# Optimization experiments

Hardware: AMD Instinct MI355X
Metric: run time of the kernel (lower is better)

The kernel has to match this reference:

```python
import jax, jax.numpy as jnp
import numpy as np
import math

N, E, F, H = 8000, 64000, 64, 10
C = F  # out_channels == in_channels in Drug's RAGCN
INV_SQRT_F = 1.0 / math.sqrt(F)


def _glorot(key, shape):
    lim = math.sqrt(6.0 / (shape[0] + shape[1]))
    return jax.random.uniform(key, shape, jnp.float32, -lim, lim)


def setup_inputs() -> dict:
    key = jax.random.key(0)
    ks = jax.random.split(key, 16)
    x = jax.random.normal(ks[0], (N, F), jnp.float32)
    edge_attr = jax.random.normal(ks[1], (E, F), jnp.float32)
    # directed edges with no self loops (module removes them before adding its own)
    src = jax.random.randint(ks[2], (E,), 0, N)
    off = jax.random.randint(ks[3], (E,), 1, N)
    dst = (src + off) % N
    edge_index = jnp.stack([src, dst]).astype(jnp.int32)
    return {
        'x': x,
        'edge_index': edge_index,
        'edge_attr': edge_attr,
        'W_src': _glorot(ks[4], (F, H * C)),
        'Wnq': _glorot(ks[5], (F, F)),
        'Wnk': _glorot(ks[6], (F, F)),
        'Wnv': _glorot(ks[7], (F, F)),
        'Weq': _glorot(ks[8], (F, F)),
        'Wev': _glorot(ks[9], (F, F)),
        'Wek': _glorot(ks[10], (F, F)),
        'W4': _glorot(ks[11], (2 * F, F)),
        'W5': _glorot(ks[12], (F, F)),
        'g1': jnp.ones((F,), jnp.float32),
        'b1': jnp.zeros((F,), jnp.float32),
        'g2': jnp.ones((F,), jnp.float32),
        'b2': jnp.zeros((F,), jnp.float32),
        'bias': jnp.zeros((H * C,), jnp.float32),
    }


def _layernorm(v, g, b):  # torch LayerNorm, eps=0, affine, biased variance
    mu = jnp.mean(v, axis=-1, keepdims=True)
    var = jnp.mean((v - mu) ** 2, axis=-1, keepdims=True)
    return (v - mu) * jax.lax.rsqrt(var) * g + b


def reference(x, edge_index, edge_attr, W_src, Wnq, Wnk, Wnv, Weq, Wev, Wek,
              W4, W5, g1, b1, g2, b2, bias):
    src, dst = edge_index[0], edge_index[1]
    # add_self_loops with fill_value='mean': loop attr = mean of incoming edge_attr
    deg = jax.ops.segment_sum(jnp.ones((E,), x.dtype), dst, num_segments=N)
    loop_attr = jax.ops.segment_sum(edge_attr, dst, num_segments=N) / jnp.maximum(deg, 1.0)[:, None]
    loops = jnp.arange(N, dtype=src.dtype)
    s = jnp.concatenate([src, loops])                  # [Et] edge source index
    ea = jnp.concatenate([edge_attr, loop_attr], 0)    # [Et, F]

    x_src = (x @ W_src).reshape(N, H, C)               # [N, H, C]
    x_j = x_src[s]                                     # gather: [Et, H, C]

    node_K = x_j @ Wnk
    node_V = x_j @ Wnv
    node_Q = x_src @ Wnq
    edge_K = ea @ Weq   # naming follows source: w_e_q feeds edge_K etc.
    edge_V = ea @ Wev
    edge_Q = ea @ Wek

    K_s = jax.ops.segment_sum(node_K + edge_K[:, None, :], s, num_segments=N)
    V_s = jax.ops.segment_sum(node_V + edge_V[:, None, :], s, num_segments=N)
    Q_s = jax.ops.segment_sum(edge_Q, s, num_segments=N)[:, None, :] + node_Q

    qk = jnp.einsum('nhc,nhc->nh', Q_s, K_s) * INV_SQRT_F
    alphi = jax.nn.softmax(qk, axis=1)[:, :, None] * V_s   # softmax over heads dim
    node_update = x_src * alphi                            # [N, H, C]

    # edge update branch
    xj2 = node_update[s]                                   # [Et, H, C]
    edge_rep = jnp.broadcast_to(ea[:, None, :], (s.shape[0], H, F))
    m = jax.nn.relu(jnp.concatenate([edge_rep, xj2], axis=2) @ W4)
    u = _layernorm(m @ W5 + ea[:, None, :], g1, b1)
    eu = _layernorm(u @ W5 + ea[:, None, :], g2, b2)       # source reuses w5

    node_out = node_update.reshape(N, H * C) + bias        # concat heads + bias
    edge_out = eu[:E].mean(axis=1)  # remove appended self loops, mean over heads
    return node_out, edge_out
```

## Files before the change

### kernel.cpp

```cpp
#include <hip/hip_runtime.h>
#include <cstdint>
#include <cstddef>

#define NN 8000
#define EE 64000
#define HH 10

#define OFF_W5T 0
#define OFF_WNQ 4096
#define OFF_WNQL 8192
#define OFF_WNK 12288
#define OFF_WNKL 16384
#define OFF_WNV 20480
#define OFF_WNVL 24576
#define OFF_W4B 28672
#define OFF_W4T 32768
#define OFF_WSRC 36864
#define OFF_WSRCL 77824

typedef __attribute__((ext_vector_type(8))) short bf16x8;
typedef __attribute__((ext_vector_type(4))) float f32x4;
typedef __attribute__((ext_vector_type(4))) unsigned int u32x4;

__device__ __forceinline__ int rfl(int v) { return __builtin_amdgcn_readfirstlane(v); }

__device__ __forceinline__ unsigned int rne16(float w) {
  unsigned int b = __float_as_uint(w);
  return (b + 0x7FFFu + ((b >> 16) & 1u)) >> 16;
}

__device__ __forceinline__ bf16x8 pack8(f32x4 a, f32x4 b) {
  u32x4 u;
  u[0] = (__float_as_uint(a[1]) & 0xFFFF0000u) | (__float_as_uint(a[0]) >> 16);
  u[1] = (__float_as_uint(a[3]) & 0xFFFF0000u) | (__float_as_uint(a[2]) >> 16);
  u[2] = (__float_as_uint(b[1]) & 0xFFFF0000u) | (__float_as_uint(b[0]) >> 16);
  u[3] = (__float_as_uint(b[3]) & 0xFFFF0000u) | (__float_as_uint(b[2]) >> 16);
  return __builtin_bit_cast(bf16x8, u);
}

__device__ __forceinline__ void split8(f32x4 a, f32x4 b, bf16x8& hi, bf16x8& lo) {
  unsigned int h[4], l[4];
#pragma unroll
  for (int j = 0; j < 2; ++j) {
    unsigned int b0 = __float_as_uint(a[2 * j]);
    unsigned int b1 = __float_as_uint(a[2 * j + 1]);
    h[j] = (b1 & 0xFFFF0000u) | (b0 >> 16);
    float r0 = a[2 * j] - __uint_as_float(b0 & 0xFFFF0000u);
    float r1 = a[2 * j + 1] - __uint_as_float(b1 & 0xFFFF0000u);
    l[j] = (__float_as_uint(r1) & 0xFFFF0000u) | (__float_as_uint(r0) >> 16);
  }
#pragma unroll
  for (int j = 0; j < 2; ++j) {
    unsigned int b0 = __float_as_uint(b[2 * j]);
    unsigned int b1 = __float_as_uint(b[2 * j + 1]);
    h[2 + j] = (b1 & 0xFFFF0000u) | (b0 >> 16);
    float r0 = b[2 * j] - __uint_as_float(b0 & 0xFFFF0000u);
    float r1 = b[2 * j + 1] - __uint_as_float(b1 & 0xFFFF0000u);
    l[2 + j] = (__float_as_uint(r1) & 0xFFFF0000u) | (__float_as_uint(r0) >> 16);
  }
  u32x4 uh = {h[0], h[1], h[2], h[3]};
  u32x4 ul = {l[0], l[1], l[2], l[3]};
  hi = __builtin_bit_cast(bf16x8, uh);
  lo = __builtin_bit_cast(bf16x8, ul);
}

__device__ __forceinline__ f32x4 relu4(f32x4 a, f32x4 b) {
  f32x4 o;
#pragma unroll
  for (int j = 0; j < 4; ++j) o[j] = fmaxf(a[j] + b[j], 0.f);
  return o;
}

__global__ void k_init(float* __restrict__ ws) {
  int t = blockIdx.x * 256 + threadIdx.x;
  int stride = gridDim.x * 256;
  for (int i = t; i < 130 * NN; i += stride)
    ws[i] = (i >= NN && i < 2 * NN) ? 1.0f : 0.0f;
}

__global__ void k_scatter(const int* __restrict__ ei, const float* __restrict__ ea,
                          float* __restrict__ deg, float* __restrict__ dout,
                          float* __restrict__ sum_in, float* __restrict__ sum_src) {
  int t = blockIdx.x * 256 + threadIdx.x;
  if (t >= EE * 64) return;
  int e = t >> 6, f = t & 63;
  int s = ei[e];
  int d = ei[EE + e];
  float v = ea[t];
  atomicAdd(&sum_in[d * 64 + f], v);
  atomicAdd(&sum_src[s * 64 + f], v);
  if (f == 0) {
    atomicAdd(&deg[d], 1.0f);
    atomicAdd(&dout[s], 1.0f);
  }
}

__global__ void k_prep(const float* __restrict__ W5, const float* __restrict__ g1,
                       const float* __restrict__ b1, float* __restrict__ Cg,
                       float* __restrict__ Cb, unsigned short* __restrict__ wbuf) {
  const int c = blockIdx.x;
  const int f = threadIdx.x;
  float w = W5[f * 64 + c];
  wbuf[OFF_W5T + c * 64 + f] = (unsigned short)rne16(w);
  float cg = g1[f] * w;
  float cb = b1[f] * w;
#pragma unroll
  for (int off = 1; off < 64; off <<= 1) {
    cg += __shfl_xor(cg, off, 64);
    cb += __shfl_xor(cb, off, 64);
  }
  if (f == 0) {
    Cg[c] = cg;
    Cb[c] = cb;
  }
}

__global__ void k_prepw(const float* __restrict__ Wnq, const float* __restrict__ Wnk,
                        const float* __restrict__ Wnv, const float* __restrict__ W4,
                        const float* __restrict__ Wsrc, unsigned short* __restrict__ wbuf) {
  const int c = blockIdx.x, f = threadIdx.x, y = blockIdx.y;
  float w;
  int hioff, looff = -1;
  const int cf = c * 64 + f;
  if (y == 0) { w = Wnq[f * 64 + c]; hioff = OFF_WNQ + cf; looff = OFF_WNQL + cf; }
  else if (y == 1) { w = Wnk[f * 64 + c]; hioff = OFF_WNK + cf; looff = OFF_WNKL + cf; }
  else if (y == 2) { w = Wnv[f * 64 + c]; hioff = OFF_WNV + cf; looff = OFF_WNVL + cf; }
  else if (y == 3) { w = W4[(64 + f) * 64 + c]; hioff = OFF_W4B + cf; }
  else if (y == 4) { w = W4[f * 64 + c]; hioff = OFF_W4T + cf; }
  else {
    int h = y - 5;
    w = Wsrc[f * 640 + h * 64 + c];
    hioff = OFF_WSRC + (h * 64 + c) * 64 + f;
    looff = OFF_WSRCL + (h * 64 + c) * 64 + f;
  }
  unsigned int hi = rne16(w);
  wbuf[hioff] = (unsigned short)hi;
  if (looff >= 0) {
    float rest = w - __uint_as_float(hi << 16);
    wbuf[looff] = (unsigned short)rne16(rest);
  }
}

__global__ __launch_bounds__(256) void k_am(const float* __restrict__ ea,
                                            const unsigned short* __restrict__ wbuf,
                                            float* __restrict__ A) {
  const int lane = threadIdx.x & 63;
  const int wv = rfl((int)threadIdx.x >> 6);
  const int g = lane >> 4, r = lane & 15;
  const int e = (blockIdx.x * 4 + wv) * 16 + r;
  bf16x8 wa[4][2];
#pragma unroll
  for (int mt = 0; mt < 4; ++mt)
#pragma unroll
    for (int ks = 0; ks < 2; ++ks)
      wa[mt][ks] = *reinterpret_cast<const bf16x8*>(wbuf + OFF_W4T + (16 * mt + r) * 64 +
                                                    32 * ks + 8 * g);
  const float* er = ea + (size_t)e * 64 + 8 * g;
  bf16x8 xb0 = pack8(*reinterpret_cast<const f32x4*>(er), *reinterpret_cast<const f32x4*>(er + 4));
  bf16x8 xb1 = pack8(*reinterpret_cast<const f32x4*>(er + 32), *reinterpret_cast<const f32x4*>(er + 36));
#pragma unroll
  for (int mt = 0; mt < 4; ++mt) {
    f32x4 d = {0, 0, 0, 0};
    d = __builtin_amdgcn_mfma_f32_16x16x32_bf16(wa[mt][0], xb0, d, 0, 0, 0);
    d = __builtin_amdgcn_mfma_f32_16x16x32_bf16(wa[mt][1], xb1, d, 0, 0, 0);
    *reinterpret_cast<f32x4*>(A + (size_t)e * 64 + 16 * mt + 4 * g) = d;
  }
}

__global__ __launch_bounds__(256) void k_xsrcm(const float* __restrict__ x,
                                               const unsigned short* __restrict__ wbuf,
                                               float* __restrict__ xsrc) {
  const int lane = threadIdx.x & 63;
  const int wv = rfl((int)threadIdx.x >> 6);
  const int g = lane >> 4, r = lane & 15;
  const int h = blockIdx.y;
  const int n = (blockIdx.x * 4 + wv) * 16 + r;
  bf16x8 whi[4][2], wlo[4][2];
#pragma unroll
  for (int mt = 0; mt < 4; ++mt)
#pragma unroll
    for (int ks = 0; ks < 2; ++ks) {
      const int off = (h * 64 + 16 * mt + r) * 64 + 32 * ks + 8 * g;
      whi[mt][ks] = *reinterpret_cast<const bf16x8*>(wbuf + OFF_WSRC + off);
      wlo[mt][ks] = *reinterpret_cast<const bf16x8*>(wbuf + OFF_WSRCL + off);
    }
  const float* xr = x + (size_t)n * 64 + 8 * g;
  bf16x8 xh0, xl0, xh1, xl1;
  split8(*reinterpret_cast<const f32x4*>(xr), *reinterpret_cast<const f32x4*>(xr + 4), xh0, xl0);
  split8(*reinterpret_cast<const f32x4*>(xr + 32), *reinterpret_cast<const f32x4*>(xr + 36), xh1, xl1);
  const size_t base = ((size_t)n * 10 + h) * 64;
#pragma unroll
  for (int mt = 0; mt < 4; ++mt) {
    f32x4 d = {0, 0, 0, 0};
    d = __builtin_amdgcn_mfma_f32_16x16x32_bf16(whi[mt][0], xh0, d, 0, 0, 0);
    d = __builtin_amdgcn_mfma_f32_16x16x32_bf16(whi[mt][1], xh1, d, 0, 0, 0);
    d = __builtin_amdgcn_mfma_f32_16x16x32_bf16(whi[mt][0], xl0, d, 0, 0, 0);
    d = __builtin_amdgcn_mfma_f32_16x16x32_bf16(whi[mt][1], xl1, d, 0, 0, 0);
    d = __builtin_amdgcn_mfma_f32_16x16x32_bf16(wlo[mt][0], xh0, d, 0, 0, 0);
    d = __builtin_amdgcn_mfma_f32_16x16x32_bf16(wlo[mt][1], xh1, d, 0, 0, 0);
    *reinterpret_cast<f32x4*>(xsrc + base + 16 * mt + 4 * g) = d;
  }
}

__global__ __launch_bounds__(256) void k_eaqkv(const float* __restrict__ deg,
                                               const float* __restrict__ sum_in,
                                               const float* __restrict__ sum_src,
                                               const float* __restrict__ Wek,
                                               const float* __restrict__ Weq,
                                               const float* __restrict__ Wev,
                                               float* __restrict__ eaQ,
                                               float* __restrict__ eaK,
                                               float* __restrict__ eaV) {
  const int lane = threadIdx.x & 63;
  const int wv = rfl(threadIdx.x >> 6);
  float wq[64], wk[64], wvv[64];
#pragma unroll
  for (int f = 0; f < 64; ++f) {
    wq[f] = Wek[f * 64 + lane];
// ... 99 lines not shown
    s += v[h];
  }
  float inv = 1.0f / s;
#pragma unroll
  for (int h = 0; h < HH; ++h) sm[n * HH + h] = v[h] * inv;
}

__global__ __launch_bounds__(256) void k_updm(const float* __restrict__ xsrc,
                                              const unsigned short* __restrict__ wbuf,
                                              const float* __restrict__ eaV,
                                              const float* __restrict__ dout,
                                              const float* __restrict__ sm,
                                              const float* __restrict__ bias,
                                              float* __restrict__ node_out,
                                              float* __restrict__ NB) {
  const int lane = threadIdx.x & 63;
  const int wv = rfl((int)threadIdx.x >> 6);
  const int g = lane >> 4, r = lane & 15;
  const int grow = (blockIdx.x * 4 + wv) * 16 + r;
  const int n = grow / 10;
  const int h = grow - 10 * n;
  const float* xp = xsrc + (size_t)grow * 64;
  bf16x8 xh0, xl0, xh1, xl1;
  split8(*reinterpret_cast<const f32x4*>(xp + 8 * g), *reinterpret_cast<const f32x4*>(xp + 8 * g + 4),
         xh0, xl0);
  split8(*reinterpret_cast<const f32x4*>(xp + 8 * g + 32),
         *reinterpret_cast<const f32x4*>(xp + 8 * g + 36), xh1, xl1);
  const float dn = dout[n];
  const float wgt = sm[grow];
  f32x4 nu[4];
#pragma unroll
  for (int mt = 0; mt < 4; ++mt) {
    const int off = (16 * mt + r) * 64 + 8 * g;
    bf16x8 ah0 = *reinterpret_cast<const bf16x8*>(wbuf + OFF_WNV + off);
    bf16x8 ah1 = *reinterpret_cast<const bf16x8*>(wbuf + OFF_WNV + off + 32);
    bf16x8 al0 = *reinterpret_cast<const bf16x8*>(wbuf + OFF_WNVL + off);
    bf16x8 al1 = *reinterpret_cast<const bf16x8*>(wbuf + OFF_WNVL + off + 32);
    f32x4 vf = {0, 0, 0, 0};
    vf = __builtin_amdgcn_mfma_f32_16x16x32_bf16(ah0, xh0, vf, 0, 0, 0);
    vf = __builtin_amdgcn_mfma_f32_16x16x32_bf16(ah1, xh1, vf, 0, 0, 0);
    vf = __builtin_amdgcn_mfma_f32_16x16x32_bf16(ah0, xl0, vf, 0, 0, 0);
    vf = __builtin_amdgcn_mfma_f32_16x16x32_bf16(ah1, xl1, vf, 0, 0, 0);
    vf = __builtin_amdgcn_mfma_f32_16x16x32_bf16(al0, xh0, vf, 0, 0, 0);
    vf = __builtin_amdgcn_mfma_f32_16x16x32_bf16(al1, xh1, vf, 0, 0, 0);
    f32x4 ev = *reinterpret_cast<const f32x4*>(eaV + (size_t)n * 64 + 16 * mt + 4 * g);
    f32x4 xs = *reinterpret_cast<const f32x4*>(xp + 16 * mt + 4 * g);
    f32x4 nn;
#pragma unroll
    for (int q = 0; q < 4; ++q) nn[q] = xs[q] * wgt * fmaf(dn, vf[q], ev[q]);
    nu[mt] = nn;
    f32x4 bs = *reinterpret_cast<const f32x4*>(bias + h * 64 + 16 * mt + 4 * g);
    *reinterpret_cast<f32x4*>(node_out + (size_t)grow * 64 + 16 * mt + 4 * g) = nn + bs;
  }
  const int l0 = (((2 * g) & 3) << 4) | r;
  const int l1 = (((2 * g + 1) & 3) << 4) | r;
  const bool hiHalf = (g >= 2);
  float vv[16];
#pragma unroll
  for (int ks = 0; ks < 2; ++ks)
#pragma unroll
    for (int i = 0; i < 8; ++i) {
      const int sl = (i < 4) ? l0 : l1;
      float vlo = __shfl(nu[2 * ks][i & 3], sl, 64);
      float vhi = __shfl(nu[2 * ks + 1][i & 3], sl, 64);
      vv[ks * 8 + i] = hiHalf ? vhi : vlo;
    }
  f32x4 q0 = {vv[0], vv[1], vv[2], vv[3]};
  f32x4 q1 = {vv[4], vv[5], vv[6], vv[7]};
  f32x4 q2 = {vv[8], vv[9], vv[10], vv[11]};
  f32x4 q3 = {vv[12], vv[13], vv[14], vv[15]};
  bf16x8 nb0 = pack8(q0, q1);
  bf16x8 nb1 = pack8(q2, q3);
#pragma unroll
  for (int mt = 0; mt < 4; ++mt) {
    const int off = (16 * mt + r) * 64 + 8 * g;
    bf16x8 ba0 = *reinterpret_cast<const bf16x8*>(wbuf + OFF_W4B + off);
    bf16x8 ba1 = *reinterpret_cast<const bf16x8*>(wbuf + OFF_W4B + off + 32);
    f32x4 nf = {0, 0, 0, 0};
    nf = __builtin_amdgcn_mfma_f32_16x16x32_bf16(ba0, nb0, nf, 0, 0, 0);
    nf = __builtin_amdgcn_mfma_f32_16x16x32_bf16(ba1, nb1, nf, 0, 0, 0);
    *reinterpret_cast<f32x4*>(NB + (size_t)grow * 64 + 16 * mt + 4 * g) = nf;
  }
}

__global__ __launch_bounds__(256) void k_edge5(
    const int* __restrict__ ei, const float* __restrict__ ea_g,
    const float* __restrict__ NB, const float* __restrict__ AT,
    const unsigned short* __restrict__ wbuf, const float* __restrict__ Cgp,
    const float* __restrict__ Cbp, const float* __restrict__ g1v,
    const float* __restrict__ g2v, const float* __restrict__ bias2,
    float* __restrict__ edge_out) {
  const int lane = threadIdx.x & 63;
  const int wv = rfl((int)threadIdx.x >> 6);
  const int g = lane >> 4;
  const int r = lane & 15;
  const int e = (blockIdx.x * 4 + wv) * 16 + r;
  const int src = ei[e];

  bf16x8 whi[4][2];
#pragma unroll
  for (int mt = 0; mt < 4; ++mt)
#pragma unroll
    for (int ks = 0; ks < 2; ++ks)
      whi[mt][ks] = *reinterpret_cast<const bf16x8*>(wbuf + OFF_W5T + (16 * mt + r) * 64 +
                                                     32 * ks + 8 * g);

  const float* ATr = AT + (size_t)e * 64 + 8 * g;
  f32x4 at0 = *reinterpret_cast<const f32x4*>(ATr);
  f32x4 at1 = *reinterpret_cast<const f32x4*>(ATr + 4);
  f32x4 at2 = *reinterpret_cast<const f32x4*>(ATr + 32);
  f32x4 at3 = *reinterpret_cast<const f32x4*>(ATr + 36);
  const float* EAr = ea_g + (size_t)e * 64;
  const float* NBr = NB + (size_t)src * 640 + 8 * g;

  const int l0 = (((2 * g) & 3) << 4) | r;
  const int l1 = (((2 * g + 1) & 3) << 4) | r;
  const bool hiHalf = (g >= 2);

  f32x4 outacc[4] = {{0, 0, 0, 0}, {0, 0, 0, 0}, {0, 0, 0, 0}, {0, 0, 0, 0}};

#pragma unroll 1
  for (int h = 0; h < HH; ++h) {
    const float* nb = NBr + h * 64;
    bf16x8 mhi0 = pack8(relu4(at0, *reinterpret_cast<const f32x4*>(nb)),
                        relu4(at1, *reinterpret_cast<const f32x4*>(nb + 4)));
    bf16x8 mhi1 = pack8(relu4(at2, *reinterpret_cast<const f32x4*>(nb + 32)),
                        relu4(at3, *reinterpret_cast<const f32x4*>(nb + 36)));

    f32x4 acc1[4];
#pragma unroll
    for (int mt = 0; mt < 4; ++mt) {
      f32x4 a = *reinterpret_cast<const f32x4*>(EAr + 16 * mt + 4 * g);
      a = __builtin_amdgcn_mfma_f32_16x16x32_bf16(whi[mt][0], mhi0, a, 0, 0, 0);
      a = __builtin_amdgcn_mfma_f32_16x16x32_bf16(whi[mt][1], mhi1, a, 0, 0, 0);
      acc1[mt] = a;
    }

    float s = 0.f, s2 = 0.f;
#pragma unroll
    for (int mt = 0; mt < 4; ++mt)
#pragma unroll
      for (int q = 0; q < 4; ++q) {
        float v = acc1[mt][q];
        s += v;
        s2 = fmaf(v, v, s2);
      }
    s += __shfl_xor(s, 16, 64);
    s2 += __shfl_xor(s2, 16, 64);
    s += __shfl_xor(s, 32, 64);
    s2 += __shfl_xor(s2, 32, 64);
    const float mu1 = s * 0.015625f;
    const float rs1 = rsqrtf(fmaxf(s2 * 0.015625f - mu1 * mu1, 1e-30f));

    f32x4 us[4];
#pragma unroll
    for (int mt = 0; mt < 4; ++mt) {
      f32x4 gv = *reinterpret_cast<const f32x4*>(g1v + 16 * mt + 4 * g);
      us[mt] = acc1[mt] * gv * rs1;
    }
    float vv[16];
#pragma unroll
    for (int ks = 0; ks < 2; ++ks)
#pragma unroll
      for (int i = 0; i < 8; ++i) {
        const int sl = (i < 4) ? l0 : l1;
        float vlo = __shfl(us[2 * ks][i & 3], sl, 64);
        float vhi = __shfl(us[2 * ks + 1][i & 3], sl, 64);
        vv[ks * 8 + i] = hiHalf ? vhi : vlo;
      }
    f32x4 q0 = {vv[0], vv[1], vv[2], vv[3]};
    f32x4 q1 = {vv[4], vv[5], vv[6], vv[7]};
    f32x4 q2 = {vv[8], vv[9], vv[10], vv[11]};
    f32x4 q3 = {vv[12], vv[13], vv[14], vv[15]};
    bf16x8 bhi0 = pack8(q0, q1);
    bf16x8 bhi1 = pack8(q2, q3);

    const float m1r1 = mu1 * rs1;
    f32x4 acc2[4];
#pragma unroll
    for (int mt = 0; mt < 4; ++mt) {
      f32x4 eav = *reinterpret_cast<const f32x4*>(EAr + 16 * mt + 4 * g);
      f32x4 cbv = *reinterpret_cast<const f32x4*>(Cbp + 16 * mt + 4 * g);
      f32x4 cgv = *reinterpret_cast<const f32x4*>(Cgp + 16 * mt + 4 * g);
      f32x4 a = eav + cbv - m1r1 * cgv;
      a = __builtin_amdgcn_mfma_f32_16x16x32_bf16(whi[mt][0], bhi0, a, 0, 0, 0);
      a = __builtin_amdgcn_mfma_f32_16x16x32_bf16(whi[mt][1], bhi1, a, 0, 0, 0);
      acc2[mt] = a;
    }

    float t = 0.f, t2 = 0.f;
#pragma unroll
    for (int mt = 0; mt < 4; ++mt)
#pragma unroll
      for (int q = 0; q < 4; ++q) {
        float v = acc2[mt][q];
        t += v;
        t2 = fmaf(v, v, t2);
      }
    t += __shfl_xor(t, 16, 64);
    t2 += __shfl_xor(t2, 16, 64);
    t += __shfl_xor(t, 32, 64);
    t2 += __shfl_xor(t2, 32, 64);
    const float mu2 = t * 0.015625f;
    const float rs2 = rsqrtf(fmaxf(t2 * 0.015625f - mu2 * mu2, 1e-30f));
#pragma unroll
    for (int mt = 0; mt < 4; ++mt) {
      f32x4 g2f = *reinterpret_cast<const f32x4*>(g2v + 16 * mt + 4 * g);
      f32x4 b2f = *reinterpret_cast<const f32x4*>(bias2 + 16 * mt + 4 * g);
      outacc[mt] += (acc2[mt] - mu2) * rs2 * g2f + b2f;
    }
  }

#pragma unroll
  for (int mt = 0; mt < 4; ++mt) {
    f32x4 o = outacc[mt] * 0.1f;
    *reinterpret_cast<f32x4*>(edge_out + (size_t)e * 64 + 16 * mt + 4 * g) = o;
  }
}

extern "C" void kernel_launch(void* const* d_in, const int* in_sizes, int n_in,
                              void* d_out, int out_size, void* d_ws, size_t ws_size,
                              hipStream_t stream) {
  const float* x = (const float*)d_in[0];
  const int* ei = (const int*)d_in[1];
  const float* edge_attr = (const float*)d_in[2];
  const float* W_src = (const float*)d_in[3];
  const float* Wnq = (const float*)d_in[4];
  const float* Wnk = (const float*)d_in[5];
  const float* Wnv = (const float*)d_in[6];
  const float* Weq = (const float*)d_in[7];
  const float* Wev = (const float*)d_in[8];
  const float* Wek = (const float*)d_in[9];
  const float* W4 = (const float*)d_in[10];
  const float* W5 = (const float*)d_in[11];
  const float* g1 = (const float*)d_in[12];
  const float* b1 = (const float*)d_in[13];
  const float* g2 = (const float*)d_in[14];
  const float* b2 = (const float*)d_in[15];
  const float* bias = (const float*)d_in[16];
  (void)in_sizes; (void)n_in; (void)out_size; (void)ws_size;

  float* ws = (float*)d_ws;
  float* deg = ws;
  float* dout = ws + NN;
  float* sum_in = ws + 2 * NN;
  float* sum_src = ws + 66 * NN;
  unsigned short* wbuf = (unsigned short*)(ws + 130 * NN);
  float* eaQ = ws + 194 * NN;
  float* eaK = ws + 258 * NN;
  float* eaV = ws + 322 * NN;
  float* xsrc = ws + 386 * NN;
  float* NB = ws + 1026 * NN;
  float* qk = ws + 1666 * NN;
  float* sm = ws + 1676 * NN;
  float* A = ws + 1686 * NN;
  float* Cg = ws + 1686 * NN + 64 * EE;
  float* Cb = Cg + 64;

  float* node_out = (float*)d_out;
  float* edge_out = (float*)d_out + (size_t)NN * 640;

  k_init<<<1024, 256, 0, stream>>>(ws);
  k_prep<<<64, 64, 0, stream>>>(W5, g1, b1, Cg, Cb, wbuf);
  k_prepw<<<dim3(64, 15), 64, 0, stream>>>(Wnq, Wnk, Wnv, W4, W_src, wbuf);
  k_scatter<<<EE * 64 / 256, 256, 0, stream>>>(ei, edge_attr, deg, dout, sum_in, sum_src);
  k_am<<<EE / 64, 256, 0, stream>>>(edge_attr, wbuf, A);
  k_xsrcm<<<dim3(NN / 64, 10), 256, 0, stream>>>(x, wbuf, xsrc);
  k_eaqkv<<<250, 256, 0, stream>>>(deg, sum_in, sum_src, Wek, Weq, Wev, eaQ, eaK, eaV);
  k_qkm<<<NN * HH / 64, 256, 0, stream>>>(xsrc, wbuf, eaQ, eaK, dout, qk);
  k_softmax<<<(NN + 255) / 256, 256, 0, stream>>>(qk, sm);
  k_updm<<<NN * HH / 64, 256, 0, stream>>>(xsrc, wbuf, eaV, dout, sm, bias, node_out, NB);
  k_edge5<<<EE / 64, 256, 0, stream>>>(ei, edge_attr, NB, A, wbuf, Cg, Cb, g1, g2, b2,
                                       edge_out);
}
```

Measured before the change: 188.0 us.

## Fuse edge-attr W4 projection into edge kernel, merge prep kernels, pair heads

The separate k_am kernel that wrote the ea@W4 projection to a 16 MB workspace buffer is removed. The edge kernel now computes it in registers via MFMA plus a lane exchange, cutting a global write and re-read and one launch. The two weight-prep kernels are merged into one launch. The edge kernel also processes two heads per loop iteration so independent MFMA chains interleave, at the cost of more live registers.

```diff
diff --git a/kernel.cpp b/kernel.cpp
--- a/kernel.cpp
+++ b/kernel.cpp
@@ -69,6 +69,24 @@
 #pragma unroll
   for (int j = 0; j < 4; ++j) o[j] = fmaxf(a[j] + b[j], 0.f);
   return o;
+}
+
+__device__ __forceinline__ void xchg(const f32x4 us[4], int l0, int l1, bool hiHalf,
+                                     f32x4& q0, f32x4& q1, f32x4& q2, f32x4& q3) {
+  float vv[16];
+#pragma unroll
+  for (int ks = 0; ks < 2; ++ks)
+#pragma unroll
+    for (int i = 0; i < 8; ++i) {
+      const int sl = (i < 4) ? l0 : l1;
+      float vlo = __shfl(us[2 * ks][i & 3], sl, 64);
+      float vhi = __shfl(us[2 * ks + 1][i & 3], sl, 64);
+      vv[ks * 8 + i] = hiHalf ? vhi : vlo;
+    }
+  q0 = {vv[0], vv[1], vv[2], vv[3]};
+  q1 = {vv[4], vv[5], vv[6], vv[7]};
+  q2 = {vv[8], vv[9], vv[10], vv[11]};
+  q3 = {vv[12], vv[13], vv[14], vv[15]};
 }
 
 __global__ void k_init(float* __restrict__ ws) {
@@ -95,30 +113,29 @@
   }
 }
 
-__global__ void k_prep(const float* __restrict__ W5, const float* __restrict__ g1,
-                       const float* __restrict__ b1, float* __restrict__ Cg,
-                       float* __restrict__ Cb, unsigned short* __restrict__ wbuf) {
-  const int c = blockIdx.x;
-  const int f = threadIdx.x;
-  float w = W5[f * 64 + c];
-  wbuf[OFF_W5T + c * 64 + f] = (unsigned short)rne16(w);
-  float cg = g1[f] * w;
-  float cb = b1[f] * w;
-#pragma unroll
-  for (int off = 1; off < 64; off <<= 1) {
-    cg += __shfl_xor(cg, off, 64);
-    cb += __shfl_xor(cb, off, 64);
-  }
-  if (f == 0) {
-    Cg[c] = cg;
-    Cb[c] = cb;
-  }
-}
-
-__global__ void k_prepw(const float* __restrict__ Wnq, const float* __restrict__ Wnk,
-                        const float* __restrict__ Wnv, const float* __restrict__ W4,
-                        const float* __restrict__ Wsrc, unsigned short* __restrict__ wbuf) {
+__global__ void k_prepall(const float* __restrict__ Wnq, const float* __restrict__ Wnk,
+                          const float* __restrict__ Wnv, const float* __restrict__ W4,
+                          const float* __restrict__ Wsrc, const float* __restrict__ W5,
+                          const float* __restrict__ g1, const float* __restrict__ b1,
+                          float* __restrict__ Cg, float* __restrict__ Cb,
+                          unsigned short* __restrict__ wbuf) {
   const int c = blockIdx.x, f = threadIdx.x, y = blockIdx.y;
+  if (y == 15) {
+    float w = W5[f * 64 + c];
+    wbuf[OFF_W5T + c * 64 + f] = (unsigned short)rne16(w);
+    float cg = g1[f] * w;
+    float cb = b1[f] * w;
+#pragma unroll
+    for (int off = 1; off < 64; off <<= 1) {
+      cg += __shfl_xor(cg, off, 64);
+      cb += __shfl_xor(cb, off, 64);
+    }
+    if (f == 0) {
+      Cg[c] = cg;
+      Cb[c] = cb;
+    }
+    return;
+  }
   float w;
   int hioff, looff = -1;
   const int cf = c * 64 + f;
@@ -138,32 +155,6 @@
   if (looff >= 0) {
     float rest = w - __uint_as_float(hi << 16);
     wbuf[looff] = (unsigned short)rne16(rest);
-  }
-}
-
-__global__ __launch_bounds__(256) void k_am(const float* __restrict__ ea,
-                                            const unsigned short* __restrict__ wbuf,
-                                            float* __restrict__ A) {
-  const int lane = threadIdx.x & 63;
-  const int wv = rfl((int)threadIdx.x >> 6);
-  const int g = lane >> 4, r = lane & 15;
-  const int e = (blockIdx.x * 4 + wv) * 16 + r;
-  bf16x8 wa[4][2];
-#pragma unroll
-  for (int mt = 0; mt < 4; ++mt)
-#pragma unroll
-    for (int ks = 0; ks < 2; ++ks)
-      wa[mt][ks] = *reinterpret_cast<const bf16x8*>(wbuf + OFF_W4T + (16 * mt + r) * 64 +
-                                                    32 * ks + 8 * g);
-  const float* er = ea + (size_t)e * 64 + 8 * g;
-  bf16x8 xb0 = pack8(*reinterpret_cast<const f32x4*>(er), *reinterpret_cast<const f32x4*>(er + 4));
-  bf16x8 xb1 = pack8(*reinterpret_cast<const f32x4*>(er + 32), *reinterpret_cast<const f32x4*>(er + 36));
-#pragma unroll
-  for (int mt = 0; mt < 4; ++mt) {
-    f32x4 d = {0, 0, 0, 0};
-    d = __builtin_amdgcn_mfma_f32_16x16x32_bf16(wa[mt][0], xb0, d, 0, 0, 0);
-    d = __builtin_amdgcn_mfma_f32_16x16x32_bf16(wa[mt][1], xb1, d, 0, 0, 0);
-    *reinterpret_cast<f32x4*>(A + (size_t)e * 64 + 16 * mt + 4 * g) = d;
   }
 }
 
@@ -372,20 +363,8 @@
   const int l0 = (((2 * g) & 3) << 4) | r;
   const int l1 = (((2 * g + 1) & 3) << 4) | r;
   const bool hiHalf = (g >= 2);
-  float vv[16];
-#pragma unroll
-  for (int ks = 0; ks < 2; ++ks)
-#pragma unroll
-    for (int i = 0; i < 8; ++i) {
-      const int sl = (i < 4) ? l0 : l1;
-      float vlo = __shfl(nu[2 * ks][i & 3], sl, 64);
-      float vhi = __shfl(nu[2 * ks + 1][i & 3], sl, 64);
-      vv[ks * 8 + i] = hiHalf ? vhi : vlo;
-    }
-  f32x4 q0 = {vv[0], vv[1], vv[2], vv[3]};
-  f32x4 q1 = {vv[4], vv[5], vv[6], vv[7]};
-  f32x4 q2 = {vv[8], vv[9], vv[10], vv[11]};
-  f32x4 q3 = {vv[12], vv[13], vv[14], vv[15]};
+  f32x4 q0, q1, q2, q3;
+  xchg(nu, l0, l1, hiHalf, q0, q1, q2, q3);
   bf16x8 nb0 = pack8(q0, q1);
   bf16x8 nb1 = pack8(q2, q3);
 #pragma unroll
@@ -400,19 +379,21 @@
   }
 }
 
-__global__ __launch_bounds__(256) void k_edge5(
+__global__ __launch_bounds__(256) void k_edge6(
     const int* __restrict__ ei, const float* __restrict__ ea_g,
-    const float* __restrict__ NB, const float* __restrict__ AT,
-    const unsigned short* __restrict__ wbuf, const float* __restrict__ Cgp,
-    const float* __restrict__ Cbp, const float* __restrict__ g1v,
-    const float* __restrict__ g2v, const float* __restrict__ bias2,
-    float* __restrict__ edge_out) {
+    const float* __restrict__ NB, const unsigned short* __restrict__ wbuf,
+    const float* __restrict__ Cgp, const float* __restrict__ Cbp,
+    const float* __restrict__ g1v, const float* __restrict__ g2v,
+    const float* __restrict__ bias2, float* __restrict__ edge_out) {
   const int lane = threadIdx.x & 63;
   const int wv = rfl((int)threadIdx.x >> 6);
   const int g = lane >> 4;
   const int r = lane & 15;
   const int e = (blockIdx.x * 4 + wv) * 16 + r;
   const int src = ei[e];
+  const int l0 = (((2 * g) & 3) << 4) | r;
+  const int l1 = (((2 * g + 1) & 3) << 4) | r;
+  const bool hiHalf = (g >= 2);
 
   bf16x8 whi[4][2];
 #pragma unroll
@@ -422,109 +403,125 @@
       whi[mt][ks] = *reinterpret_cast<const bf16x8*>(wbuf + OFF_W5T + (16 * mt + r) * 64 +
                                                      32 * ks + 8 * g);
 
-  const float* ATr = AT + (size_t)e * 64 + 8 * g;
-  f32x4 at0 = *reinterpret_cast<const f32x4*>(ATr);
-  f32x4 at1 = *reinterpret_cast<const f32x4*>(ATr + 4);
-  f32x4 at2 = *reinterpret_cast<const f32x4*>(ATr + 32);
-  f32x4 at3 = *reinterpret_cast<const f32x4*>(ATr + 36);
   const float* EAr = ea_g + (size_t)e * 64;
+  const float* ear = EAr + 8 * g;
+
+  f32x4 at0, at1, at2, at3;
+  {
+    bf16x8 eb0 = pack8(*reinterpret_cast<const f32x4*>(ear),
+                       *reinterpret_cast<const f32x4*>(ear + 4));
+    bf16x8 eb1 = pack8(*reinterpret_cast<const f32x4*>(ear + 32),
+                       *reinterpret_cast<const f32x4*>(ear + 36));
+    f32x4 ad[4];
+#pragma unroll
+    for (int mt = 0; mt < 4; ++mt) {
+      const int off = (16 * mt + r) * 64 + 8 * g;
+      bf16x8 w0 = *reinterpret_cast<const bf16x8*>(wbuf + OFF_W4T + off);
+      bf16x8 w1 = *reinterpret_cast<const bf16x8*>(wbuf + OFF_W4T + off + 32);
+      f32x4 d = {0, 0, 0, 0};
+      d = __builtin_amdgcn_mfma_f32_16x16x32_bf16(w0, eb0, d, 0, 0, 0);
+      d = __builtin_amdgcn_mfma_f32_16x16x32_bf16(w1, eb1, d, 0, 0, 0);
+      ad[mt] = d;
+    }
+    xchg(ad, l0, l1, hiHalf, at0, at1, at2, at3);
+  }
+
   const float* NBr = NB + (size_t)src * 640 + 8 * g;
-
-  const int l0 = (((2 * g) & 3) << 4) | r;
-  const int l1 = (((2 * g + 1) & 3) << 4) | r;
-  const bool hiHalf = (g >= 2);
-
   f32x4 outacc[4] = {{0, 0, 0, 0}, {0, 0, 0, 0}, {0, 0, 0, 0}, {0, 0, 0, 0}};
 
 #pragma unroll 1
-  for (int h = 0; h < HH; ++h) {
-    const float* nb = NBr + h * 64;
-    bf16x8 mhi0 = pack8(relu4(at0, *reinterpret_cast<const f32x4*>(nb)),
-                        relu4(at1, *reinterpret_cast<const f32x4*>(nb + 4)));
-    bf16x8 mhi1 = pack8(relu4(at2, *reinterpret_cast<const f32x4*>(nb + 32)),
-                        relu4(at3, *reinterpret_cast<const f32x4*>(nb + 36)));
-
-    f32x4 acc1[4];
+  for (int hp = 0; hp < 5; ++hp) {
+    const float* nbA = NBr + (2 * hp) * 64;
+    const float* nbB = nbA + 64;
+    bf16x8 mA0 = pack8(relu4(at0, *reinterpret_cast<const f32x4*>(nbA)),
+                       relu4(at1, *reinterpret_cast<const f32x4*>(nbA + 4)));
+    bf16x8 mA1 = pack8(relu4(at2, *reinterpret_cast<const f32x4*>(nbA + 32)),
+                       relu4(at3, *reinterpret_cast<const f32x4*>(nbA + 36)));
+    bf16x8 mB0 = pack8(relu4(at0, *reinterpret_cast<const f32x4*>(nbB)),
+                       relu4(at1, *reinterpret_cast<const f32x4*>(nbB + 4)));
+    bf16x8 mB1 = pack8(relu4(at2, *reinterpret_cast<const f32x4*>(nbB + 32)),
+                       relu4(at3, *reinterpret_cast<const f32x4*>(nbB + 36)));
+
+    f32x4 aA[4], aB[4];
 #pragma unroll
     for (int mt = 0; mt < 4; ++mt) {
-      f32x4 a = *reinterpret_cast<const f32x4*>(EAr + 16 * mt + 4 * g);
-      a = __builtin_amdgcn_mfma_f32_16x16x32_bf16(whi[mt][0], mhi0, a, 0, 0, 0);
-      a = __builtin_amdgcn_mfma_f32_16x16x32_bf16(whi[mt][1], mhi1, a, 0, 0, 0);
-      acc1[mt] = a;
-    }
-
-    float s = 0.f, s2 = 0.f;
+      f32x4 c = *reinterpret_cast<const f32x4*>(EAr + 16 * mt + 4 * g);
+      f32x4 dA = __builtin_amdgcn_mfma_f32_16x16x32_bf16(whi[mt][0], mA0, c, 0, 0, 0);
+      f32x4 dB = __builtin_amdgcn_mfma_f32_16x16x32_bf16(whi[mt][0], mB0, c, 0, 0, 0);
+      dA = __builtin_amdgcn_mfma_f32_16x16x32_bf16(whi[mt][1], mA1, dA, 0, 0, 0);
+      dB = __builtin_amdgcn_mfma_f32_16x16x32_bf16(whi[mt][1], mB1, dB, 0, 0, 0);
+      aA[mt] = dA;
+      aB[mt] = dB;
+    }
+
+    float sA = 0.f, s2A = 0.f, sB = 0.f, s2B = 0.f;
 #pragma unroll
     for (int mt = 0; mt < 4; ++mt)
 #pragma unroll
       for (int q = 0; q < 4; ++q) {
-        float v = acc1[mt][q];
-        s += v;
-        s2 = fmaf(v, v, s2);
+        float vA = aA[mt][q], vB = aB[mt][q];
+        sA += vA; s2A = fmaf(vA, vA, s2A);
+        sB += vB; s2B = fmaf(vB, vB, s2B);
       }
-    s += __shfl_xor(s, 16, 64);
-    s2 += __shfl_xor(s2, 16, 64);
-    s += __shfl_xor(s, 32, 64);
-    s2 += __shfl_xor(s2, 32, 64);
-    const float mu1 = s * 0.015625f;
-    const float rs1 = rsqrtf(fmaxf(s2 * 0.015625f - mu1 * mu1, 1e-30f));
-
-    f32x4 us[4];
+    sA += __shfl_xor(sA, 16, 64); sB += __shfl_xor(sB, 16, 64);
+    s2A += __shfl_xor(s2A, 16, 64); s2B += __shfl_xor(s2B, 16, 64);
+    sA += __shfl_xor(sA, 32, 64); sB += __shfl_xor(sB, 32, 64);
+    s2A += __shfl_xor(s2A, 32, 64); s2B += __shfl_xor(s2B, 32, 64);
+    const float muA = sA * 0.015625f, muB = sB * 0.015625f;
+    const float rsA = rsqrtf(fmaxf(s2A * 0.015625f - muA * muA, 1e-30f));
+    const float rsB = rsqrtf(fmaxf(s2B * 0.015625f - muB * muB, 1e-30f));
+
 #pragma unroll
     for (int mt = 0; mt < 4; ++mt) {
       f32x4 gv = *reinterpret_cast<const f32x4*>(g1v + 16 * mt + 4 * g);
-      us[mt] = acc1[mt] * gv * rs1;
-    }
-    float vv[16];
-#pragma unroll
-    for (int ks = 0; ks < 2; ++ks)
-#pragma unroll
-      for (int i = 0; i < 8; ++i) {
-        const int sl = (i < 4) ? l0 : l1;
-        float vlo = __shfl(us[2 * ks][i & 3], sl, 64);
-        float vhi = __shfl(us[2 * ks + 1][i & 3], sl, 64);
-        vv[ks * 8 + i] = hiHalf ? vhi : vlo;
-      }
-    f32x4 q0 = {vv[0], vv[1], vv[2], vv[3]};
-    f32x4 q1 = {vv[4], vv[5], vv[6], vv[7]};
-    f32x4 q2 = {vv[8], vv[9], vv[10], vv[11]};
-    f32x4 q3 = {vv[12], vv[13], vv[14], vv[15]};
-    bf16x8 bhi0 = pack8(q0, q1);
-    bf16x8 bhi1 = pack8(q2, q3);
-
-    const float m1r1 = mu1 * rs1;
-    f32x4 acc2[4];
+      aA[mt] = aA[mt] * gv * rsA;
+      aB[mt] = aB[mt] * gv * rsB;
+    }
+    f32x4 qA0, qA1, qA2, qA3, qB0, qB1, qB2, qB3;
+    xchg(aA, l0, l1, hiHalf, qA0, qA1, qA2, qA3);
+    xchg(aB, l0, l1, hiHalf, qB0, qB1, qB2, qB3);
+    bf16x8 bA0 = pack8(qA0, qA1), bA1 = pack8(qA2, qA3);
+    bf16x8 bB0 = pack8(qB0, qB1), bB1 = pack8(qB2, qB3);
+
+    const float mrA = muA * rsA, mrB = muB * rsB;
 #pragma unroll
     for (int mt = 0; mt < 4; ++mt) {
       f32x4 eav = *reinterpret_cast<const f32x4*>(EAr + 16 * mt + 4 * g);
       f32x4 cbv = *reinterpret_cast<const f32x4*>(Cbp + 16 * mt + 4 * g);
       f32x4 cgv = *reinterpret_cast<const f32x4*>(Cgp + 16 * mt + 4 * g);
-      f32x4 a = eav + cbv - m1r1 * cgv;
-      a = __builtin_amdgcn_mfma_f32_16x16x32_bf16(whi[mt][0], bhi0, a, 0, 0, 0);
-      a = __builtin_amdgcn_mfma_f32_16x16x32_bf16(whi[mt][1], bhi1, a, 0, 0, 0);
-      acc2[mt] = a;
-    }
-
-    float t = 0.f, t2 = 0.f;
+      f32x4 base = eav + cbv;
+      f32x4 dA = base - mrA * cgv;
+      f32x4 dB = base - mrB * cgv;
+      dA = __builtin_amdgcn_mfma_f32_16x16x32_bf16(whi[mt][0], bA0, dA, 0, 0, 0);
+      dB = __builtin_amdgcn_mfma_f32_16x16x32_bf16(whi[mt][0], bB0, dB, 0, 0, 0);
+      dA = __builtin_amdgcn_mfma_f32_16x16x32_bf16(whi[mt][1], bA1, dA, 0, 0, 0);
+      dB = __builtin_amdgcn_mfma_f32_16x16x32_bf16(whi[mt][1], bB1, dB, 0, 0, 0);
+      aA[mt] = dA;
+      aB[mt] = dB;
+    }
+
+    float tA = 0.f, t2A = 0.f, tB = 0.f, t2B = 0.f;
 #pragma unroll
     for (int mt = 0; mt < 4; ++mt)
 #pragma unroll
       for (int q = 0; q < 4; ++q) {
-        float v = acc2[mt][q];
-        t += v;
-        t2 = fmaf(v, v, t2);
+        float vA = aA[mt][q], vB = aB[mt][q];
+        tA += vA; t2A = fmaf(vA, vA, t2A);
+        tB += vB; t2B = fmaf(vB, vB, t2B);
       }
-    t += __shfl_xor(t, 16, 64);
-    t2 += __shfl_xor(t2, 16, 64);
-    t += __shfl_xor(t, 32, 64);
-    t2 += __shfl_xor(t2, 32, 64);
-    const float mu2 = t * 0.015625f;
-    const float rs2 = rsqrtf(fmaxf(t2 * 0.015625f - mu2 * mu2, 1e-30f));
+    tA += __shfl_xor(tA, 16, 64); tB += __shfl_xor(tB, 16, 64);
+    t2A += __shfl_xor(t2A, 16, 64); t2B += __shfl_xor(t2B, 16, 64);
+    tA += __shfl_xor(tA, 32, 64); tB += __shfl_xor(tB, 32, 64);
+    t2A += __shfl_xor(t2A, 32, 64); t2B += __shfl_xor(t2B, 32, 64);
+    const float m2A = tA * 0.015625f, m2B = tB * 0.015625f;
+    const float r2A = rsqrtf(fmaxf(t2A * 0.015625f - m2A * m2A, 1e-30f));
+    const float r2B = rsqrtf(fmaxf(t2B * 0.015625f - m2B * m2B, 1e-30f));
 #pragma unroll
     for (int mt = 0; mt < 4; ++mt) {
       f32x4 g2f = *reinterpret_cast<const f32x4*>(g2v + 16 * mt + 4 * g);
       f32x4 b2f = *reinterpret_cast<const f32x4*>(bias2 + 16 * mt + 4 * g);
-      outacc[mt] += (acc2[mt] - mu2) * rs2 * g2f + b2f;
+      outacc[mt] += (aA[mt] - m2A) * r2A * g2f + b2f;
+      outacc[mt] += (aB[mt] - m2B) * r2B * g2f + b2f;
     }
   }
 
@@ -570,7 +567,6 @@
   float* NB = ws + 1026 * NN;
   float* qk = ws + 1666 * NN;
   float* sm = ws + 1676 * NN;
-  float* A = ws + 1686 * NN;
   float* Cg = ws + 1686 * NN + 64 * EE;
   float* Cb = Cg + 64;
 
@@ -578,15 +574,14 @@
   float* edge_out = (float*)d_out + (size_t)NN * 640;
 
   k_init<<<1024, 256, 0, stream>>>(ws);
-  k_prep<<<64, 64, 0, stream>>>(W5, g1, b1, Cg, Cb, wbuf);
-  k_prepw<<<dim3(64, 15), 64, 0, stream>>>(Wnq, Wnk, Wnv, W4, W_src, wbuf);
+  k_prepall<<<dim3(64, 16), 64, 0, stream>>>(Wnq, Wnk, Wnv, W4, W_src, W5, g1, b1, Cg, Cb,
+                                             wbuf);
   k_scatter<<<EE * 64 / 256, 256, 0, stream>>>(ei, edge_attr, deg, dout, sum_in, sum_src);
-  k_am<<<EE / 64, 256, 0, stream>>>(edge_attr, wbuf, A);
   k_xsrcm<<<dim3(NN / 64, 10), 256, 0, stream>>>(x, wbuf, xsrc);
   k_eaqkv<<<250, 256, 0, stream>>>(deg, sum_in, sum_src, Wek, Weq, Wev, eaQ, eaK, eaV);
   k_qkm<<<NN * HH / 64, 256, 0, stream>>>(xsrc, wbuf, eaQ, eaK, dout, qk);
   k_softmax<<<(NN + 255) / 256, 256, 0, stream>>>(qk, sm);
   k_updm<<<NN * HH / 64, 256, 0, stream>>>(xsrc, wbuf, eaV, dout, sm, bias, node_out, NB);
-  k_edge5<<<EE / 64, 256, 0, stream>>>(ei, edge_attr, NB, A, wbuf, Cg, Cb, g1, g2, b2,
+  k_edge6<<<EE / 64, 256, 0, stream>>>(ei, edge_attr, NB, wbuf, Cg, Cb, g1, g2, b2,
                                        edge_out);
 }
```

Measured after the change: 185.2 us. No clear change (-1.5%).

## Fuse edge-attr W4 GEMM into edge kernel and permute weights to drop shuffles

Applied to the files above, without the earlier changes.

Drops the separate k_am kernel and its 64000x64 fp32 intermediate A. The edge_attr @ W4-top product is now recomputed with MFMA inside the edge kernel. The K dimension of W4-bottom and W5 is permuted during weight prep so that MFMA output fragments can be packed straight into the next MFMA's B operand, removing the cross-lane shuffle transposes in both k_updm and the edge kernel. The two weight-prep kernels are merged into one launch. Together these cut a launch, a large global write and read, and shuffle work, at the cost of some extra MFMA and register use in the edge kernel.

```diff
diff --git a/kernel.cpp b/kernel.cpp
--- a/kernel.cpp
+++ b/kernel.cpp
@@ -23,6 +23,10 @@
 typedef __attribute__((ext_vector_type(4))) unsigned int u32x4;
 
 __device__ __forceinline__ int rfl(int v) { return __builtin_amdgcn_readfirstlane(v); }
+
+__device__ __forceinline__ int cbperm(int k) {
+  return 32 * (k >> 5) + 16 * ((k >> 2) & 1) + 4 * ((k >> 3) & 3) + (k & 3);
+}
 
 __device__ __forceinline__ unsigned int rne16(float w) {
   unsigned int b = __float_as_uint(w);
@@ -95,37 +99,37 @@
   }
 }
 
-__global__ void k_prep(const float* __restrict__ W5, const float* __restrict__ g1,
-                       const float* __restrict__ b1, float* __restrict__ Cg,
-                       float* __restrict__ Cb, unsigned short* __restrict__ wbuf) {
-  const int c = blockIdx.x;
-  const int f = threadIdx.x;
-  float w = W5[f * 64 + c];
-  wbuf[OFF_W5T + c * 64 + f] = (unsigned short)rne16(w);
-  float cg = g1[f] * w;
-  float cb = b1[f] * w;
-#pragma unroll
-  for (int off = 1; off < 64; off <<= 1) {
-    cg += __shfl_xor(cg, off, 64);
-    cb += __shfl_xor(cb, off, 64);
-  }
-  if (f == 0) {
-    Cg[c] = cg;
-    Cb[c] = cb;
-  }
-}
-
-__global__ void k_prepw(const float* __restrict__ Wnq, const float* __restrict__ Wnk,
-                        const float* __restrict__ Wnv, const float* __restrict__ W4,
-                        const float* __restrict__ Wsrc, unsigned short* __restrict__ wbuf) {
+__global__ void k_prepall(const float* __restrict__ Wnq, const float* __restrict__ Wnk,
+                          const float* __restrict__ Wnv, const float* __restrict__ W4,
+                          const float* __restrict__ Wsrc, const float* __restrict__ W5,
+                          const float* __restrict__ g1, const float* __restrict__ b1,
+                          float* __restrict__ Cg, float* __restrict__ Cb,
+                          unsigned short* __restrict__ wbuf) {
   const int c = blockIdx.x, f = threadIdx.x, y = blockIdx.y;
+  if (y == 15) {
+    const int cb = cbperm(f);
+    float w = W5[cb * 64 + c];
+    wbuf[OFF_W5T + c * 64 + f] = (unsigned short)rne16(w);
+    float cg = g1[cb] * w;
+    float cbb = b1[cb] * w;
+#pragma unroll
+    for (int off = 1; off < 64; off <<= 1) {
+      cg += __shfl_xor(cg, off, 64);
+      cbb += __shfl_xor(cbb, off, 64);
+    }
+    if (f == 0) {
+      Cg[c] = cg;
+      Cb[c] = cbb;
+    }
+    return;
+  }
   float w;
   int hioff, looff = -1;
   const int cf = c * 64 + f;
   if (y == 0) { w = Wnq[f * 64 + c]; hioff = OFF_WNQ + cf; looff = OFF_WNQL + cf; }
   else if (y == 1) { w = Wnk[f * 64 + c]; hioff = OFF_WNK + cf; looff = OFF_WNKL + cf; }
   else if (y == 2) { w = Wnv[f * 64 + c]; hioff = OFF_WNV + cf; looff = OFF_WNVL + cf; }
-  else if (y == 3) { w = W4[(64 + f) * 64 + c]; hioff = OFF_W4B + cf; }
+  else if (y == 3) { w = W4[(64 + cbperm(f)) * 64 + c]; hioff = OFF_W4B + cf; }
   else if (y == 4) { w = W4[f * 64 + c]; hioff = OFF_W4T + cf; }
   else {
     int h = y - 5;
@@ -138,32 +142,6 @@
   if (looff >= 0) {
     float rest = w - __uint_as_float(hi << 16);
     wbuf[looff] = (unsigned short)rne16(rest);
-  }
-}
-
-__global__ __launch_bounds__(256) void k_am(const float* __restrict__ ea,
-                                            const unsigned short* __restrict__ wbuf,
-                                            float* __restrict__ A) {
-  const int lane = threadIdx.x & 63;
-  const int wv = rfl((int)threadIdx.x >> 6);
-  const int g = lane >> 4, r = lane & 15;
-  const int e = (blockIdx.x * 4 + wv) * 16 + r;
-  bf16x8 wa[4][2];
-#pragma unroll
-  for (int mt = 0; mt < 4; ++mt)
-#pragma unroll
-    for (int ks = 0; ks < 2; ++ks)
-      wa[mt][ks] = *reinterpret_cast<const bf16x8*>(wbuf + OFF_W4T + (16 * mt + r) * 64 +
-                                                    32 * ks + 8 * g);
-  const float* er = ea + (size_t)e * 64 + 8 * g;
-  bf16x8 xb0 = pack8(*reinterpret_cast<const f32x4*>(er), *reinterpret_cast<const f32x4*>(er + 4));
-  bf16x8 xb1 = pack8(*reinterpret_cast<const f32x4*>(er + 32), *reinterpret_cast<const f32x4*>(er + 36));
-#pragma unroll
-  for (int mt = 0; mt < 4; ++mt) {
-    f32x4 d = {0, 0, 0, 0};
-    d = __builtin_amdgcn_mfma_f32_16x16x32_bf16(wa[mt][0], xb0, d, 0, 0, 0);
-    d = __builtin_amdgcn_mfma_f32_16x16x32_bf16(wa[mt][1], xb1, d, 0, 0, 0);
-    *reinterpret_cast<f32x4*>(A + (size_t)e * 64 + 16 * mt + 4 * g) = d;
   }
 }
 
@@ -369,25 +347,8 @@
     f32x4 bs = *reinterpret_cast<const f32x4*>(bias + h * 64 + 16 * mt + 4 * g);
     *reinterpret_cast<f32x4*>(node_out + (size_t)grow * 64 + 16 * mt + 4 * g) = nn + bs;
   }
-  const int l0 = (((2 * g) & 3) << 4) | r;
-  const int l1 = (((2 * g + 1) & 3) << 4) | r;
-  const bool hiHalf = (g >= 2);
-  float vv[16];
-#pragma unroll
-  for (int ks = 0; ks < 2; ++ks)
-#pragma unroll
-    for (int i = 0; i < 8; ++i) {
-      const int sl = (i < 4) ? l0 : l1;
-      float vlo = __shfl(nu[2 * ks][i & 3], sl, 64);
-      float vhi = __shfl(nu[2 * ks + 1][i & 3], sl, 64);
-      vv[ks * 8 + i] = hiHalf ? vhi : vlo;
-    }
-  f32x4 q0 = {vv[0], vv[1], vv[2], vv[3]};
-  f32x4 q1 = {vv[4], vv[5], vv[6], vv[7]};
-  f32x4 q2 = {vv[8], vv[9], vv[10], vv[11]};
-  f32x4 q3 = {vv[12], vv[13], vv[14], vv[15]};
-  bf16x8 nb0 = pack8(q0, q1);
-  bf16x8 nb1 = pack8(q2, q3);
+  bf16x8 nb0 = pack8(nu[0], nu[1]);
+  bf16x8 nb1 = pack8(nu[2], nu[3]);
 #pragma unroll
   for (int mt = 0; mt < 4; ++mt) {
     const int off = (16 * mt + r) * 64 + 8 * g;
@@ -400,13 +361,12 @@
   }
 }
 
-__global__ __launch_bounds__(256) void k_edge5(
+__global__ __launch_bounds__(256) void k_edge7(
     const int* __restrict__ ei, const float* __restrict__ ea_g,
-    const float* __restrict__ NB, const float* __restrict__ AT,
-    const unsigned short* __restrict__ wbuf, const float* __restrict__ Cgp,
-    const float* __restrict__ Cbp, const float* __restrict__ g1v,
-    const float* __restrict__ g2v, const float* __restrict__ bias2,
-    float* __restrict__ edge_out) {
+    const float* __restrict__ NB, const unsigned short* __restrict__ wbuf,
+    const float* __restrict__ Cgp, const float* __restrict__ Cbp,
+    const float* __restrict__ g1v, const float* __restrict__ g2v,
+    const float* __restrict__ bias2, float* __restrict__ edge_out) {
   const int lane = threadIdx.x & 63;
   const int wv = rfl((int)threadIdx.x >> 6);
   const int g = lane >> 4;
@@ -422,34 +382,46 @@
       whi[mt][ks] = *reinterpret_cast<const bf16x8*>(wbuf + OFF_W5T + (16 * mt + r) * 64 +
                                                      32 * ks + 8 * g);
 
-  const float* ATr = AT + (size_t)e * 64 + 8 * g;
-  f32x4 at0 = *reinterpret_cast<const f32x4*>(ATr);
-  f32x4 at1 = *reinterpret_cast<const f32x4*>(ATr + 4);
-  f32x4 at2 = *reinterpret_cast<const f32x4*>(ATr + 32);
-  f32x4 at3 = *reinterpret_cast<const f32x4*>(ATr + 36);
   const float* EAr = ea_g + (size_t)e * 64;
-  const float* NBr = NB + (size_t)src * 640 + 8 * g;
-
-  const int l0 = (((2 * g) & 3) << 4) | r;
-  const int l1 = (((2 * g + 1) & 3) << 4) | r;
-  const bool hiHalf = (g >= 2);
-
+  const float* ear = EAr + 8 * g;
+
+  f32x4 ad[4];
+  {
+    bf16x8 eb0 = pack8(*reinterpret_cast<const f32x4*>(ear),
+                       *reinterpret_cast<const f32x4*>(ear + 4));
+    bf16x8 eb1 = pack8(*reinterpret_cast<const f32x4*>(ear + 32),
+                       *reinterpret_cast<const f32x4*>(ear + 36));
+#pragma unroll
+    for (int mt = 0; mt < 4; ++mt) {
+      const int off = (16 * mt + r) * 64 + 8 * g;
+      bf16x8 w0 = *reinterpret_cast<const bf16x8*>(wbuf + OFF_W4T + off);
+      bf16x8 w1 = *reinterpret_cast<const bf16x8*>(wbuf + OFF_W4T + off + 32);
+      f32x4 d = {0, 0, 0, 0};
+      d = __builtin_amdgcn_mfma_f32_16x16x32_bf16(w0, eb0, d, 0, 0, 0);
+      d = __builtin_amdgcn_mfma_f32_16x16x32_bf16(w1, eb1, d, 0, 0, 0);
+      ad[mt] = d;
+    }
+  }
+
+  const float* NBr = NB + (size_t)src * 640;
   f32x4 outacc[4] = {{0, 0, 0, 0}, {0, 0, 0, 0}, {0, 0, 0, 0}, {0, 0, 0, 0}};
 
 #pragma unroll 1
   for (int h = 0; h < HH; ++h) {
     const float* nb = NBr + h * 64;
-    bf16x8 mhi0 = pack8(relu4(at0, *reinterpret_cast<const f32x4*>(nb)),
-                        relu4(at1, *reinterpret_cast<const f32x4*>(nb + 4)));
-    bf16x8 mhi1 = pack8(relu4(at2, *reinterpret_cast<const f32x4*>(nb + 32)),
-                        relu4(at3, *reinterpret_cast<const f32x4*>(nb + 36)));
+    f32x4 n0 = *reinterpret_cast<const f32x4*>(nb + 4 * g);
+    f32x4 n1 = *reinterpret_cast<const f32x4*>(nb + 16 + 4 * g);
+    f32x4 n2 = *reinterpret_cast<const f32x4*>(nb + 32 + 4 * g);
+    f32x4 n3 = *reinterpret_cast<const f32x4*>(nb + 48 + 4 * g);
+    bf16x8 bhi0 = pack8(relu4(ad[0], n0), relu4(ad[1], n1));
+    bf16x8 bhi1 = pack8(relu4(ad[2], n2), relu4(ad[3], n3));
 
     f32x4 acc1[4];
 #pragma unroll
     for (int mt = 0; mt < 4; ++mt) {
       f32x4 a = *reinterpret_cast<const f32x4*>(EAr + 16 * mt + 4 * g);
-      a = __builtin_amdgcn_mfma_f32_16x16x32_bf16(whi[mt][0], mhi0, a, 0, 0, 0);
-      a = __builtin_amdgcn_mfma_f32_16x16x32_bf16(whi[mt][1], mhi1, a, 0, 0, 0);
+      a = __builtin_amdgcn_mfma_f32_16x16x32_bf16(whi[mt][0], bhi0, a, 0, 0, 0);
+      a = __builtin_amdgcn_mfma_f32_16x16x32_bf16(whi[mt][1], bhi1, a, 0, 0, 0);
       acc1[mt] = a;
     }
 
@@ -469,28 +441,13 @@
     const float mu1 = s * 0.015625f;
     const float rs1 = rsqrtf(fmaxf(s2 * 0.015625f - mu1 * mu1, 1e-30f));
 
-    f32x4 us[4];
 #pragma unroll
     for (int mt = 0; mt < 4; ++mt) {
       f32x4 gv = *reinterpret_cast<const f32x4*>(g1v + 16 * mt + 4 * g);
-      us[mt] = acc1[mt] * gv * rs1;
-    }
-    float vv[16];
-#pragma unroll
-    for (int ks = 0; ks < 2; ++ks)
-#pragma unroll
-      for (int i = 0; i < 8; ++i) {
-        const int sl = (i < 4) ? l0 : l1;
-        float vlo = __shfl(us[2 * ks][i & 3], sl, 64);
-        float vhi = __shfl(us[2 * ks + 1][i & 3], sl, 64);
-        vv[ks * 8 + i] = hiHalf ? vhi : vlo;
-      }
-    f32x4 q0 = {vv[0], vv[1], vv[2], vv[3]};
-    f32x4 q1 = {vv[4], vv[5], vv[6], vv[7]};
-    f32x4 q2 = {vv[8], vv[9], vv[10], vv[11]};
-    f32x4 q3 = {vv[12], vv[13], vv[14], vv[15]};
-    bf16x8 bhi0 = pack8(q0, q1);
-    bf16x8 bhi1 = pack8(q2, q3);
+      acc1[mt] = acc1[mt] * gv * rs1;
+    }
+    bf16x8 b20 = pack8(acc1[0], acc1[1]);
+    bf16x8 b21 = pack8(acc1[2], acc1[3]);
 
     const float m1r1 = mu1 * rs1;
     f32x4 acc2[4];
@@ -500,8 +457,8 @@
       f32x4 cbv = *reinterpret_cast<const f32x4*>(Cbp + 16 * mt + 4 * g);
       f32x4 cgv = *reinterpret_cast<const f32x4*>(Cgp + 16 * mt + 4 * g);
       f32x4 a = eav + cbv - m1r1 * cgv;
-      a = __builtin_amdgcn_mfma_f32_16x16x32_bf16(whi[mt][0], bhi0, a, 0, 0, 0);
-      a = __builtin_amdgcn_mfma_f32_16x16x32_bf16(whi[mt][1], bhi1, a, 0, 0, 0);
+      a = __builtin_amdgcn_mfma_f32_16x16x32_bf16(whi[mt][0], b20, a, 0, 0, 0);
+      a = __builtin_amdgcn_mfma_f32_16x16x32_bf16(whi[mt][1], b21, a, 0, 0, 0);
       acc2[mt] = a;
     }
 
@@ -570,7 +527,6 @@
   float* NB = ws + 1026 * NN;
   float* qk = ws + 1666 * NN;
   float* sm = ws + 1676 * NN;
-  float* A = ws + 1686 * NN;
   float* Cg = ws + 1686 * NN + 64 * EE;
   float* Cb = Cg + 64;
 
@@ -578,15 +534,14 @@
   float* edge_out = (float*)d_out + (size_t)NN * 640;
 
   k_init<<<1024, 256, 0, stream>>>(ws);
-  k_prep<<<64, 64, 0, stream>>>(W5, g1, b1, Cg, Cb, wbuf);
-  k_prepw<<<dim3(64, 15), 64, 0, stream>>>(Wnq, Wnk, Wnv, W4, W_src, wbuf);
+  k_prepall<<<dim3(64, 16), 64, 0, stream>>>(Wnq, Wnk, Wnv, W4, W_src, W5, g1, b1, Cg, Cb,
+                                             wbuf);
   k_scatter<<<EE * 64 / 256, 256, 0, stream>>>(ei, edge_attr, deg, dout, sum_in, sum_src);
-  k_am<<<EE / 64, 256, 0, stream>>>(edge_attr, wbuf, A);
   k_xsrcm<<<dim3(NN / 64, 10), 256, 0, stream>>>(x, wbuf, xsrc);
   k_eaqkv<<<250, 256, 0, stream>>>(deg, sum_in, sum_src, Wek, Weq, Wev, eaQ, eaK, eaV);
   k_qkm<<<NN * HH / 64, 256, 0, stream>>>(xsrc, wbuf, eaQ, eaK, dout, qk);
   k_softmax<<<(NN + 255) / 256, 256, 0, stream>>>(qk, sm);
   k_updm<<<NN * HH / 64, 256, 0, stream>>>(xsrc, wbuf, eaV, dout, sm, bias, node_out, NB);
-  k_edge5<<<EE / 64, 256, 0, stream>>>(ei, edge_attr, NB, A, wbuf, Cg, Cb, g1, g2, b2,
+  k_edge7<<<EE / 64, 256, 0, stream>>>(ei, edge_attr, NB, wbuf, Cg, Cb, g1, g2, b2,
                                        edge_out);
 }
```

Measured after the change: 174.2 us. -7.3%, faster.
